# Kernel optimization log

Measured on AMD Instinct MI355X. Metric: run time of the kernel, lower is better.

The kernel has to match this reference:

```python
import jax, jax.numpy as jnp
import numpy as np

A, B, SDIM, ADIM, H, NH, DH = 15, 32768, 128, 32, 128, 4, 32
NEG = -1e9

def _lrelu(x):
    return jax.nn.leaky_relu(x, 0.01)

def setup_inputs() -> dict:
    key = jax.random.key(0)
    ks = jax.random.split(key, 14)
    w = lambda k, shp, s=0.05: jax.random.normal(k, shp, dtype=jnp.float32) * s
    return {
        'states': jax.random.normal(ks[0], (A, B, SDIM), dtype=jnp.float32),
        'actions': jax.random.normal(ks[1], (A, B, ADIM), dtype=jnp.float32),
        'Wenc': w(ks[2], (A, SDIM + ADIM, H)),
        'benc': w(ks[3], (A, H)),
        'Wsenc': w(ks[4], (A, SDIM, H)),
        'bsenc': w(ks[5], (A, H)),
        'Wk': w(ks[6], (NH, H, DH)),
        'Wsel': w(ks[7], (NH, H, DH)),
        'Wv': w(ks[8], (NH, H, DH)),
        'bv': w(ks[9], (NH, DH)),
        'Wc1': w(ks[10], (A, 2 * H, H)),
        'bc1': w(ks[11], (A, H)),
        'Wc2': w(ks[12], (A, H, ADIM)),
        'bc2': w(ks[13], (A, ADIM)),
    }

def reference(states, actions, Wenc, benc, Wsenc, bsenc, Wk, Wsel, Wv, bv, Wc1, bc1, Wc2, bc2):
    # per-agent (obs, act) encoders: [A,B,idim] x [A,idim,H] -> [A,B,H]
    sa = jnp.concatenate([states, actions], axis=-1)
    sa_enc = _lrelu(jnp.einsum('abi,aih->abh', sa, Wenc) + benc[:, None, :])
    s_enc = _lrelu(jnp.einsum('abs,ash->abh', states, Wsenc) + bsenc[:, None, :])
    # per-head key/value/selector projections (shared across agents)
    keys = jnp.einsum('jbe,ned->jbnd', sa_enc, Wk)                      # [A,B,NH,DH]
    vals = _lrelu(jnp.einsum('jbe,ned->jbnd', sa_enc, Wv) + bv[None, None])
    sel = jnp.einsum('ibe,ned->ibnd', s_enc, Wsel)                      # [A,B,NH,DH]
    # exclude-self attention over other agents
    logits = jnp.einsum('ibnd,jbnd->ibnj', sel, keys) / np.sqrt(DH).astype(np.float32)
    self_mask = jnp.eye(A, dtype=bool)[:, None, None, :]                # [A,1,1,A]
    probs = jax.nn.softmax(jnp.where(self_mask, NEG, logits), axis=-1)  # [A,B,NH,A]
    attn = jnp.einsum('ibnj,jbnd->ibnd', probs, vals)                   # [A,B,NH,DH]
    # per-agent critic head: cat(s_enc, all-head attention values) -> Q over actions
    critic_in = jnp.concatenate([s_enc, attn.reshape(A, B, NH * DH)], axis=-1)  # [A,B,2H]
    h = _lrelu(jnp.einsum('abi,aih->abh', critic_in, Wc1) + bc1[:, None, :])
    all_q = jnp.einsum('abh,aho->abo', h, Wc2) + bc2[:, None, :]        # [A,B,ADIM]
    return all_q
```

## Files before the change

kernel.cpp:

```cpp
#include <hip/hip_runtime.h>

typedef unsigned short u16;
typedef __attribute__((ext_vector_type(8))) short short8;
typedef __attribute__((ext_vector_type(4))) float f32x4;

#define NAG 15
#define NB 32768
#define NEG_BIG -1e30f

__device__ __forceinline__ u16 f2bf(float x){
  unsigned int u = __float_as_uint(x);
  u += 0x7fffu + ((u >> 16) & 1u);
  return (u16)(u >> 16);
}
__device__ __forceinline__ float bf2f(short h){
  return __uint_as_float(((unsigned int)(u16)h) << 16);
}

__global__ __launch_bounds__(256) void k0_conv(
    const float* __restrict__ Wenc, const float* __restrict__ Wsenc,
    const float* __restrict__ Wk, const float* __restrict__ Wsel, const float* __restrict__ Wv,
    const float* __restrict__ Wc1, const float* __restrict__ Wc2,
    u16* __restrict__ WencB, u16* __restrict__ WsencB,
    u16* __restrict__ WkB, u16* __restrict__ WvB, u16* __restrict__ WselB,
    u16* __restrict__ Wc1B, u16* __restrict__ Wc2B)
{
  int idx = blockIdx.x * 256 + threadIdx.x;
  if (idx < 307200){
    int a = idx / 20480, r = idx % 20480, n = r / 160, k = r % 160;
    WencB[idx] = f2bf(Wenc[a*20480 + k*128 + n]);
  } else if (idx < 552960){
    int i = idx - 307200; int a = i / 16384, r = i % 16384, n = r / 128, k = r % 128;
    WsencB[i] = f2bf(Wsenc[a*16384 + k*128 + n]);
  } else if (idx < 569344){
    int i = idx - 552960; int c = i / 128, k = i % 128;
    WkB[i] = f2bf(Wk[(c>>5)*4096 + k*32 + (c&31)]);
  } else if (idx < 585728){
    int i = idx - 569344; int c = i / 128, k = i % 128;
    WvB[i] = f2bf(Wv[(c>>5)*4096 + k*32 + (c&31)]);
  } else if (idx < 602112){
    int i = idx - 585728; int c = i / 128, k = i % 128;
    WselB[i] = f2bf(Wsel[(c>>5)*4096 + k*32 + (c&31)]);
  } else if (idx < 1093632){
    int i = idx - 602112; int a = i / 32768, r = i % 32768, n = r / 256, k = r % 256;
    Wc1B[i] = f2bf(Wc1[a*32768 + k*128 + n]);
  } else if (idx < 1155072){
    int i = idx - 1093632; int a = i / 4096, r = i % 4096, n = r / 128, k = r % 128;
    Wc2B[i] = f2bf(Wc2[a*4096 + k*32 + n]);
  }
}

__device__ __forceinline__ void mfma_block(const char* lds, int aOff, int aStride, int aMask,
    const u16* __restrict__ B, int bld, int ksteps,
    int m0, int c0, int l15, int l4, f32x4 acc[4][2])
{
  for (int ks = 0; ks < ksteps; ++ks){
    short8 af[4];
    #pragma unroll
    for (int fm = 0; fm < 4; ++fm){
      int row = m0 + fm*16 + l15;
      int slot = ks*4 + l4;
      af[fm] = *(const short8*)(lds + aOff + row*aStride + ((slot ^ (row & aMask)) << 4));
    }
    short8 bf[2];
    #pragma unroll
    for (int fn = 0; fn < 2; ++fn){
      int n = c0 + fn*16 + l15;
      bf[fn] = *(const short8*)(B + (size_t)n*bld + ks*32 + l4*8);
    }
    #pragma unroll
    for (int fm = 0; fm < 4; ++fm)
      #pragma unroll
      for (int fn = 0; fn < 2; ++fn)
        acc[fm][fn] = __builtin_amdgcn_mfma_f32_16x16x32_bf16(af[fm], bf[fn], acc[fm][fn], 0, 0, 0);
  }
}

__device__ __forceinline__ void epi_store(char* lds, f32x4 acc[4][2], const float* __restrict__ bias,
    bool act, int m0, int c0, int l15, int l4, int swzOff, int linOff)
{
  #pragma unroll
  for (int fm = 0; fm < 4; ++fm)
  #pragma unroll
  for (int fn = 0; fn < 2; ++fn){
    int col = c0 + fn*16 + l15;
    float bb = bias ? bias[col] : 0.0f;
    #pragma unroll
    for (int q = 0; q < 4; ++q){
      int row = m0 + fm*16 + l4*4 + q;
      float v = acc[fm][fn][q] + bb;
      if (act) v = v > 0.0f ? v : 0.01f * v;
      u16 h = f2bf(v);
      if (swzOff >= 0) *(u16*)(lds + swzOff + row*256 + (((col>>3) ^ (row&7))<<4) + ((col&7)<<1)) = h;
      if (linOff >= 0) *(u16*)(lds + linOff + row*256 + col*2) = h;
    }
  }
}

__device__ __forceinline__ void copy_out_bf16(const char* lds, int off, u16* __restrict__ dst,
                                              int a, int b0, int t)
{
  #pragma unroll
  for (int it = 0; it < 4; ++it){
    int e = t + it*512;
    int row = e >> 4, cb = e & 15;
    *(short8*)(dst + ((size_t)a*NB + b0 + row)*128 + cb*8) =
        *(const short8*)(lds + off + row*256 + cb*16);
  }
}

#define S_OFF 0
#define AC_OFF 32768
#define SA_OFF 40960
#define SE_OFF 73728
#define K1_LDS 106496

__global__ __launch_bounds__(512) void k1_enc(
    const float* __restrict__ states, const float* __restrict__ actions,
    const float* __restrict__ benc, const float* __restrict__ bsenc, const float* __restrict__ bvp,
    const u16* __restrict__ WencB, const u16* __restrict__ WsencB,
    const u16* __restrict__ WkB, const u16* __restrict__ WvB, const u16* __restrict__ WselB,
    u16* __restrict__ senc_g, u16* __restrict__ keys_g, u16* __restrict__ vals_g, u16* __restrict__ sel_g)
{
  extern __shared__ __align__(16) char lds[];
  const int a = blockIdx.y;
  const int b0 = blockIdx.x * 128;
  const int t = threadIdx.x;
  const int lane = t & 63, w = t >> 6;
  const int m0 = (w >> 2) * 64, c0 = (w & 3) * 32;
  const int l15 = lane & 15, l4 = lane >> 4;

  #pragma unroll
  for (int it = 0; it < 4; ++it){
    int e = t + it*512, row = e >> 4, cb = e & 15;
    const float* sp = states + ((size_t)a*NB + b0 + row)*128 + cb*8;
    float4 v0 = *(const float4*)sp, v1 = *(const float4*)(sp + 4);
    short8 p;
    p[0]=(short)f2bf(v0.x); p[1]=(short)f2bf(v0.y); p[2]=(short)f2bf(v0.z); p[3]=(short)f2bf(v0.w);
    p[4]=(short)f2bf(v1.x); p[5]=(short)f2bf(v1.y); p[6]=(short)f2bf(v1.z); p[7]=(short)f2bf(v1.w);
    *(short8*)(lds + S_OFF + row*256 + ((cb ^ (row&7))<<4)) = p;
  }
  {
    int row = t >> 2, cb = t & 3;
    const float* ap = actions + ((size_t)a*NB + b0 + row)*32 + cb*8;
    float4 v0 = *(const float4*)ap, v1 = *(const float4*)(ap + 4);
    short8 p;
    p[0]=(short)f2bf(v0.x); p[1]=(short)f2bf(v0.y); p[2]=(short)f2bf(v0.z); p[3]=(short)f2bf(v0.w);
    p[4]=(short)f2bf(v1.x); p[5]=(short)f2bf(v1.y); p[6]=(short)f2bf(v1.z); p[7]=(short)f2bf(v1.w);
    *(short8*)(lds + AC_OFF + row*64 + ((cb ^ (row&3))<<4)) = p;
  }
  __syncthreads();

  f32x4 acc[4][2];

  #pragma unroll
  for (int fm = 0; fm < 4; ++fm){ acc[fm][0] = (f32x4)0.0f; acc[fm][1] = (f32x4)0.0f; }
  mfma_block(lds, S_OFF, 256, 7, WencB + (size_t)a*20480, 160, 4, m0, c0, l15, l4, acc);
  {
    short8 af[4];
    #pragma unroll
    for (int fm = 0; fm < 4; ++fm){
      int row = m0 + fm*16 + l15;
      af[fm] = *(const short8*)(lds + AC_OFF + row*64 + ((l4 ^ (row&3))<<4));
    }
    short8 bf[2];
    #pragma unroll
    for (int fn = 0; fn < 2; ++fn){
      int n = c0 + fn*16 + l15;
      bf[fn] = *(const short8*)(WencB + (size_t)a*20480 + (size_t)n*160 + 128 + l4*8);
    }
    #pragma unroll
    for (int fm = 0; fm < 4; ++fm)
      #pragma unroll
      for (int fn = 0; fn < 2; ++fn)
        acc[fm][fn] = __builtin_amdgcn_mfma_f32_16x16x32_bf16(af[fm], bf[fn], acc[fm][fn], 0, 0, 0);
  }
  epi_store(lds, acc, benc + a*128, true, m0, c0, l15, l4, SA_OFF, -1);
  __syncthreads();

  #pragma unroll
  for (int fm = 0; fm < 4; ++fm){ acc[fm][0] = (f32x4)0.0f; acc[fm][1] = (f32x4)0.0f; }
  mfma_block(lds, S_OFF, 256, 7, WsencB + (size_t)a*16384, 128, 4, m0, c0, l15, l4, acc);
  __syncthreads();
  epi_store(lds, acc, bsenc + a*128, true, m0, c0, l15, l4, SE_OFF, 0);
  __syncthreads();
  copy_out_bf16(lds, 0, senc_g, a, b0, t);
  __syncthreads();

  #pragma unroll
  for (int fm = 0; fm < 4; ++fm){ acc[fm][0] = (f32x4)0.0f; acc[fm][1] = (f32x4)0.0f; }
  mfma_block(lds, SA_OFF, 256, 7, WkB, 128, 4, m0, c0, l15, l4, acc);
  epi_store(lds, acc, (const float*)nullptr, false, m0, c0, l15, l4, -1, 0);
  __syncthreads();
  copy_out_bf16(lds, 0, keys_g, a, b0, t);
  __syncthreads();

  #pragma unroll
  for (int fm = 0; fm < 4; ++fm){ acc[fm][0] = (f32x4)0.0f; acc[fm][1] = (f32x4)0.0f; }
  mfma_block(lds, SA_OFF, 256, 7, WvB, 128, 4, m0, c0, l15, l4, acc);
  epi_store(lds, acc, bvp, true, m0, c0, l15, l4, -1, 0);
  __syncthreads();
  copy_out_bf16(lds, 0, vals_g, a, b0, t);
  __syncthreads();

  #pragma unroll
  for (int fm = 0; fm < 4; ++fm){ acc[fm][0] = (f32x4)0.0f; acc[fm][1] = (f32x4)0.0f; }
  mfma_block(lds, SE_OFF, 256, 7, WselB, 128, 4, m0, c0, l15, l4, acc);
  epi_store(lds, acc, (const float*)nullptr, false, m0, c0, l15, l4, -1, 0);
  __syncthreads();
  copy_out_bf16(lds, 0, sel_g, a, b0, t);
}

#define K2A_LDS 130560

__global__ __launch_bounds__(512) void k2a_attn(
    const u16* __restrict__ keys_g, const u16* __restrict__ vals_g,
    const u16* __restrict__ sel_g, u16* __restrict__ attn_g)
{
  extern __shared__ __align__(16) char lds[];
  const int b0 = blockIdx.x * 16;
  const int t = threadIdx.x;
  for (int it = 0; it < 8; ++it){
    int e = t + it*512;
    if (e < 3840){
      int j = e >> 8, r = (e >> 4) & 15, c = e & 15;
      size_t src = ((size_t)j*NB + b0 + r)*128 + c*8;
      int dst = (j*16 + r)*272 + c*16;
      *(short8*)(lds + dst) = *(const short8*)(keys_g + src);
      *(short8*)(lds + 65280 + dst) = *(const short8*)(vals_g + src);
    }
  }
  __syncthreads();
  for (int e = t; e < 960; e += 512){
    int b = e & 15, n = (e >> 4) & 3, i = e >> 6;
    size_t base = ((size_t)i*NB + b0 + b)*128 + n*32;
    float sf[32];
    #pragma unroll
    for (int c4 = 0; c4 < 4; ++c4){
      short8 s8 = *(const short8*)(sel_g + base + c4*8);
      #pragma unroll
      for (int x = 0; x < 8; ++x) sf[c4*8+x] = bf2f(s8[x]);
    }
    float lg[15]; float mx = NEG_BIG;
    #pragma unroll
    for (int j = 0; j < 15; ++j){
      if (j == i){ lg[j] = NEG_BIG; continue; }
      int kb = (j*16 + b)*272 + n*64;
      float d = 0.f;
      #pragma unroll
      for (int c4 = 0; c4 < 4; ++c4){
        short8 k8 = *(const short8*)(lds + kb + c4*16);
        #pragma unroll
        for (int x = 0; x < 8; ++x) d += bf2f(k8[x]) * sf[c4*8+x];
      }
      d *= 0.17677669529663687f;
      lg[j] = d; mx = fmaxf(mx, d);
    }
    float sum = 0.f;
    #pragma unroll
    for (int j = 0; j < 15; ++j){
      float p = (j == i) ? 0.f : __expf(lg[j] - mx);
      lg[j] = p; sum += p;
    }
    float inv = 1.0f / sum;
    float oacc[32];
    #pragma unroll
    for (int x = 0; x < 32; ++x) oacc[x] = 0.f;
    #pragma unroll
    for (int j = 0; j < 15; ++j){
      if (j == i) continue;
      float p = lg[j];
      int vb = 65280 + (j*16 + b)*272 + n*64;
      #pragma unroll
      for (int c4 = 0; c4 < 4; ++c4){
        short8 v8 = *(const short8*)(lds + vb + c4*16);
        #pragma unroll
        for (int x = 0; x < 8; ++x) oacc[c4*8+x] += p * bf2f(v8[x]);
      }
    }
    #pragma unroll
    for (int c4 = 0; c4 < 4; ++c4){
      short8 o;
      #pragma unroll
      for (int x = 0; x < 8; ++x) o[x] = (short)f2bf(oacc[c4*8+x] * inv);
      *(short8*)(attn_g + base + c4*8) = o;
    }
  }
}

#define AIN_OFF 0
#define HL_OFF 65536
#define O2_OFF 98304
#define K2B_LDS 114688

__global__ __launch_bounds__(512) void k2b_critic(
    const u16* __restrict__ senc_g, const u16* __restrict__ attn_g,
    const u16* __restrict__ Wc1B, const u16* __restrict__ Wc2B,
    const float* __restrict__ bc1, const float* __restrict__ bc2,
    float* __restrict__ outp)
{
  extern __shared__ __align__(16) char lds[];
  const int a = blockIdx.y, b0 = blockIdx.x * 128, t = threadIdx.x;
  const int lane = t & 63, w = t >> 6;
  const int m0 = (w >> 2)*64, c0 = (w & 3)*32;
  const int l15 = lane & 15, l4 = lane >> 4;

  #pragma unroll
  for (int it = 0; it < 4; ++it){
    int e = t + it*512, row = e >> 4, cb = e & 15;
    size_t src = ((size_t)a*NB + b0 + row)*128 + cb*8;
    short8 v = *(const short8*)(senc_g + src);
    *(short8*)(lds + AIN_OFF + row*512 + ((cb ^ (row&7))<<4)) = v;
    short8 v2 = *(const short8*)(attn_g + src);
    *(short8*)(lds + AIN_OFF + row*512 + (((16 + cb) ^ (row&7))<<4)) = v2;
  }
  __syncthreads();

  f32x4 acc[4][2];
  #pragma unroll
  for (int fm = 0; fm < 4; ++fm){ acc[fm][0] = (f32x4)0.0f; acc[fm][1] = (f32x4)0.0f; }
  mfma_block(lds, AIN_OFF, 512, 7, Wc1B + (size_t)a*32768, 256, 8, m0, c0, l15, l4, acc);
  epi_store(lds, acc, bc1 + a*128, true, m0, c0, l15, l4, HL_OFF, -1);
  __syncthreads();

  const int r0 = (w >> 1)*32, cq = (w & 1)*16;
  f32x4 aq[2]; aq[0] = (f32x4)0.0f; aq[1] = (f32x4)0.0f;
  for (int ks = 0; ks < 4; ++ks){
    short8 af[2];
    #pragma unroll
    for (int fm = 0; fm < 2; ++fm){
      int row = r0 + fm*16 + l15, slot = ks*4 + l4;
      af[fm] = *(const short8*)(lds + HL_OFF + row*256 + ((slot ^ (row&7))<<4));
    }
    int n = cq + l15;
    short8 bq = *(const short8*)(Wc2B + (size_t)a*4096 + (size_t)n*128 + ks*32 + l4*8);
    aq[0] = __builtin_amdgcn_mfma_f32_16x16x32_bf16(af[0], bq, aq[0], 0, 0, 0);
    aq[1] = __builtin_amdgcn_mfma_f32_16x16x32_bf16(af[1], bq, aq[1], 0, 0, 0);
  }
  {
    int col = cq + l15; float bb = bc2[a*32 + col];
    #pragma unroll
    for (int fm = 0; fm < 2; ++fm)
      #pragma unroll
      for (int q = 0; q < 4; ++q){
        int row = r0 + fm*16 + l4*4 + q;
        *(float*)(lds + O2_OFF + (row*32 + col)*4) = aq[fm][q] + bb;
      }
  }
  __syncthreads();
  #pragma unroll
  for (int it = 0; it < 2; ++it){
    int e = t + it*512;
    float4 v = *(const float4*)(lds + O2_OFF + e*16);
    *(float4*)(outp + ((size_t)a*NB + b0 + (e>>3))*32 + (e&7)*4) = v;
  }
}

extern "C" void kernel_launch(void* const* d_in, const int* in_sizes, int n_in,
                              void* d_out, int out_size, void* d_ws, size_t ws_size,
                              hipStream_t stream)
{
  const float* states  = (const float*)d_in[0];
  const float* actions = (const float*)d_in[1];
  const float* Wenc    = (const float*)d_in[2];
  const float* benc    = (const float*)d_in[3];
  const float* Wsenc   = (const float*)d_in[4];
  const float* bsenc   = (const float*)d_in[5];
  const float* Wk      = (const float*)d_in[6];
  const float* Wsel    = (const float*)d_in[7];
  const float* Wv      = (const float*)d_in[8];
  const float* bv      = (const float*)d_in[9];
  const float* Wc1     = (const float*)d_in[10];
  const float* bc1     = (const float*)d_in[11];
  const float* Wc2     = (const float*)d_in[12];
  const float* bc2     = (const float*)d_in[13];

  char* ws = (char*)d_ws;
  u16* WencB  = (u16*)(ws + 0);
  u16* WsencB = (u16*)(ws + 614400);
  u16* WkB    = (u16*)(ws + 1105920);
  u16* WvB    = (u16*)(ws + 1138688);
  u16* WselB  = (u16*)(ws + 1171456);
  u16* Wc1B   = (u16*)(ws + 1204224);
  u16* Wc2B   = (u16*)(ws + 2187264);
  u16* senc_g = (u16*)(ws + 2310144);
  u16* keys_g = (u16*)(ws + 128139264);
  u16* vals_g = (u16*)(ws + 253968384);
  u16* sel_g  = (u16*)(ws + 379797504);
  if (ws_size < 505626624ULL) return;

  hipFuncSetAttribute((const void*)k1_enc,     hipFuncAttributeMaxDynamicSharedMemorySize, K1_LDS);
  hipFuncSetAttribute((const void*)k2a_attn,   hipFuncAttributeMaxDynamicSharedMemorySize, K2A_LDS);
  hipFuncSetAttribute((const void*)k2b_critic, hipFuncAttributeMaxDynamicSharedMemorySize, K2B_LDS);

  k0_conv<<<4512, 256, 0, stream>>>(Wenc, Wsenc, Wk, Wsel, Wv, Wc1, Wc2,
                                    WencB, WsencB, WkB, WvB, WselB, Wc1B, Wc2B);
  k1_enc<<<dim3(256, 15), 512, K1_LDS, stream>>>(states, actions, benc, bsenc, bv,
                                                 WencB, WsencB, WkB, WvB, WselB,
                                                 senc_g, keys_g, vals_g, sel_g);
  k2a_attn<<<2048, 512, K2A_LDS, stream>>>(keys_g, vals_g, sel_g, keys_g);
  k2b_critic<<<dim3(256, 15), 512, K2B_LDS, stream>>>(senc_g, keys_g, Wc1B, Wc2B,
                                                      bc1, bc2, (float*)d_out);
}
```

Measured before the change: 714.3 us.

## Fuse encoder, attention and critic into one kernel per 16-sample tile

Replaces the three-kernel pipeline (encoders, attention, critic) with a single kernel. Each 1024-thread block handles 16 batch rows across all 15 agents and keeps encodings, per-head keys, values, selectors and attention outputs in LDS. This removes roughly 500MB of bf16 intermediate global writes and reads. In exchange, weights are reloaded per small tile from global or L2, the block uses about 150KB of LDS (limiting occupancy), and the per-head loop adds many block barriers.

```diff
diff --git a/kernel.cpp b/kernel.cpp
--- a/kernel.cpp
+++ b/kernel.cpp
@@ -4,9 +4,7 @@
 typedef __attribute__((ext_vector_type(8))) short short8;
 typedef __attribute__((ext_vector_type(4))) float f32x4;
 
-#define NAG 15
 #define NB 32768
-#define NEG_BIG -1e30f
 
 __device__ __forceinline__ u16 f2bf(float x){
   unsigned int u = __float_as_uint(x);
@@ -15,6 +13,12 @@
 }
 __device__ __forceinline__ float bf2f(short h){
   return __uint_as_float(((unsigned int)(u16)h) << 16);
+}
+__device__ __forceinline__ short8 pack8(float4 a, float4 b){
+  short8 p;
+  p[0]=(short)f2bf(a.x); p[1]=(short)f2bf(a.y); p[2]=(short)f2bf(a.z); p[3]=(short)f2bf(a.w);
+  p[4]=(short)f2bf(b.x); p[5]=(short)f2bf(b.y); p[6]=(short)f2bf(b.z); p[7]=(short)f2bf(b.w);
+  return p;
 }
 
 __global__ __launch_bounds__(256) void k0_conv(
@@ -50,309 +54,291 @@
   }
 }
 
-__device__ __forceinline__ void mfma_block(const char* lds, int aOff, int aStride, int aMask,
-    const u16* __restrict__ B, int bld, int ksteps,
-    int m0, int c0, int l15, int l4, f32x4 acc[4][2])
-{
-  for (int ks = 0; ks < ksteps; ++ks){
-    short8 af[4];
-    #pragma unroll
-    for (int fm = 0; fm < 4; ++fm){
-      int row = m0 + fm*16 + l15;
-      int slot = ks*4 + l4;
-      af[fm] = *(const short8*)(lds + aOff + row*aStride + ((slot ^ (row & aMask)) << 4));
-    }
-    short8 bf[2];
-    #pragma unroll
-    for (int fn = 0; fn < 2; ++fn){
-      int n = c0 + fn*16 + l15;
-      bf[fn] = *(const short8*)(B + (size_t)n*bld + ks*32 + l4*8);
-    }
-    #pragma unroll
-    for (int fm = 0; fm < 4; ++fm)
-      #pragma unroll
-      for (int fn = 0; fn < 2; ++fn)
-        acc[fm][fn] = __builtin_amdgcn_mfma_f32_16x16x32_bf16(af[fm], bf[fn], acc[fm][fn], 0, 0, 0);
-  }
-}
-
-__device__ __forceinline__ void epi_store(char* lds, f32x4 acc[4][2], const float* __restrict__ bias,
-    bool act, int m0, int c0, int l15, int l4, int swzOff, int linOff)
-{
-  #pragma unroll
-  for (int fm = 0; fm < 4; ++fm)
-  #pragma unroll
-  for (int fn = 0; fn < 2; ++fn){
-    int col = c0 + fn*16 + l15;
-    float bb = bias ? bias[col] : 0.0f;
-    #pragma unroll
-    for (int q = 0; q < 4; ++q){
-      int row = m0 + fm*16 + l4*4 + q;
-      float v = acc[fm][fn][q] + bb;
-      if (act) v = v > 0.0f ? v : 0.01f * v;
-      u16 h = f2bf(v);
-      if (swzOff >= 0) *(u16*)(lds + swzOff + row*256 + (((col>>3) ^ (row&7))<<4) + ((col&7)<<1)) = h;
-      if (linOff >= 0) *(u16*)(lds + linOff + row*256 + col*2) = h;
-    }
-  }
-}
-
-__device__ __forceinline__ void copy_out_bf16(const char* lds, int off, u16* __restrict__ dst,
-                                              int a, int b0, int t)
-{
-  #pragma unroll
-  for (int it = 0; it < 4; ++it){
-    int e = t + it*512;
-    int row = e >> 4, cb = e & 15;
-    *(short8*)(dst + ((size_t)a*NB + b0 + row)*128 + cb*8) =
-        *(const short8*)(lds + off + row*256 + cb*16);
-  }
-}
-
-#define S_OFF 0
-#define AC_OFF 32768
-#define SA_OFF 40960
-#define SE_OFF 73728
-#define K1_LDS 106496
-
-__global__ __launch_bounds__(512) void k1_enc(
+#define R1 0
+#define R2 61440
+#define P1 122880
+#define P2 138240
+#define R3 122880
+#define K_LDS 153600
+
+__device__ __forceinline__ short8 ldA(const char* lds, int off, int row, int slot){
+  return *(const short8*)(lds + off + row*256 + ((slot ^ (row & 7)) << 4));
+}
+__device__ __forceinline__ void stSwz(char* lds, int off, int row, int col, u16 v){
+  *(u16*)(lds + off + row*256 + ((((col>>3) ^ (row&7))) << 4) + ((col&7) << 1)) = v;
+}
+
+#define MFMA(a8,b8,c) __builtin_amdgcn_mfma_f32_16x16x32_bf16(a8, b8, c, 0, 0, 0)
+
+__global__ __launch_bounds__(1024) void k_fused(
     const float* __restrict__ states, const float* __restrict__ actions,
     const float* __restrict__ benc, const float* __restrict__ bsenc, const float* __restrict__ bvp,
+    const float* __restrict__ bc1, const float* __restrict__ bc2,
     const u16* __restrict__ WencB, const u16* __restrict__ WsencB,
     const u16* __restrict__ WkB, const u16* __restrict__ WvB, const u16* __restrict__ WselB,
-    u16* __restrict__ senc_g, u16* __restrict__ keys_g, u16* __restrict__ vals_g, u16* __restrict__ sel_g)
-{
-  extern __shared__ __align__(16) char lds[];
-  const int a = blockIdx.y;
-  const int b0 = blockIdx.x * 128;
-  const int t = threadIdx.x;
-  const int lane = t & 63, w = t >> 6;
-  const int m0 = (w >> 2) * 64, c0 = (w & 3) * 32;
-  const int l15 = lane & 15, l4 = lane >> 4;
-
-  #pragma unroll
-  for (int it = 0; it < 4; ++it){
-    int e = t + it*512, row = e >> 4, cb = e & 15;
-    const float* sp = states + ((size_t)a*NB + b0 + row)*128 + cb*8;
-    float4 v0 = *(const float4*)sp, v1 = *(const float4*)(sp + 4);
-    short8 p;
-    p[0]=(short)f2bf(v0.x); p[1]=(short)f2bf(v0.y); p[2]=(short)f2bf(v0.z); p[3]=(short)f2bf(v0.w);
-    p[4]=(short)f2bf(v1.x); p[5]=(short)f2bf(v1.y); p[6]=(short)f2bf(v1.z); p[7]=(short)f2bf(v1.w);
-    *(short8*)(lds + S_OFF + row*256 + ((cb ^ (row&7))<<4)) = p;
-  }
-  {
-    int row = t >> 2, cb = t & 3;
-    const float* ap = actions + ((size_t)a*NB + b0 + row)*32 + cb*8;
-    float4 v0 = *(const float4*)ap, v1 = *(const float4*)(ap + 4);
-    short8 p;
-    p[0]=(short)f2bf(v0.x); p[1]=(short)f2bf(v0.y); p[2]=(short)f2bf(v0.z); p[3]=(short)f2bf(v0.w);
-    p[4]=(short)f2bf(v1.x); p[5]=(short)f2bf(v1.y); p[6]=(short)f2bf(v1.z); p[7]=(short)f2bf(v1.w);
-    *(short8*)(lds + AC_OFF + row*64 + ((cb ^ (row&3))<<4)) = p;
-  }
-  __syncthreads();
-
-  f32x4 acc[4][2];
-
-  #pragma unroll
-  for (int fm = 0; fm < 4; ++fm){ acc[fm][0] = (f32x4)0.0f; acc[fm][1] = (f32x4)0.0f; }
-  mfma_block(lds, S_OFF, 256, 7, WencB + (size_t)a*20480, 160, 4, m0, c0, l15, l4, acc);
-  {
-    short8 af[4];
-    #pragma unroll
-    for (int fm = 0; fm < 4; ++fm){
-      int row = m0 + fm*16 + l15;
-      af[fm] = *(const short8*)(lds + AC_OFF + row*64 + ((l4 ^ (row&3))<<4));
-    }
-    short8 bf[2];
-    #pragma unroll
-    for (int fn = 0; fn < 2; ++fn){
-      int n = c0 + fn*16 + l15;
-      bf[fn] = *(const short8*)(WencB + (size_t)a*20480 + (size_t)n*160 + 128 + l4*8);
-    }
-    #pragma unroll
-    for (int fm = 0; fm < 4; ++fm)
-      #pragma unroll
-      for (int fn = 0; fn < 2; ++fn)
-        acc[fm][fn] = __builtin_amdgcn_mfma_f32_16x16x32_bf16(af[fm], bf[fn], acc[fm][fn], 0, 0, 0);
-  }
-  epi_store(lds, acc, benc + a*128, true, m0, c0, l15, l4, SA_OFF, -1);
-  __syncthreads();
-
-  #pragma unroll
-  for (int fm = 0; fm < 4; ++fm){ acc[fm][0] = (f32x4)0.0f; acc[fm][1] = (f32x4)0.0f; }
-  mfma_block(lds, S_OFF, 256, 7, WsencB + (size_t)a*16384, 128, 4, m0, c0, l15, l4, acc);
-  __syncthreads();
-  epi_store(lds, acc, bsenc + a*128, true, m0, c0, l15, l4, SE_OFF, 0);
-  __syncthreads();
-  copy_out_bf16(lds, 0, senc_g, a, b0, t);
-  __syncthreads();
-
-  #pragma unroll
-  for (int fm = 0; fm < 4; ++fm){ acc[fm][0] = (f32x4)0.0f; acc[fm][1] = (f32x4)0.0f; }
-  mfma_block(lds, SA_OFF, 256, 7, WkB, 128, 4, m0, c0, l15, l4, acc);
-  epi_store(lds, acc, (const float*)nullptr, false, m0, c0, l15, l4, -1, 0);
-  __syncthreads();
-  copy_out_bf16(lds, 0, keys_g, a, b0, t);
-  __syncthreads();
-
-  #pragma unroll
-  for (int fm = 0; fm < 4; ++fm){ acc[fm][0] = (f32x4)0.0f; acc[fm][1] = (f32x4)0.0f; }
-  mfma_block(lds, SA_OFF, 256, 7, WvB, 128, 4, m0, c0, l15, l4, acc);
-  epi_store(lds, acc, bvp, true, m0, c0, l15, l4, -1, 0);
-  __syncthreads();
-  copy_out_bf16(lds, 0, vals_g, a, b0, t);
-  __syncthreads();
-
-  #pragma unroll
-  for (int fm = 0; fm < 4; ++fm){ acc[fm][0] = (f32x4)0.0f; acc[fm][1] = (f32x4)0.0f; }
-  mfma_block(lds, SE_OFF, 256, 7, WselB, 128, 4, m0, c0, l15, l4, acc);
-  epi_store(lds, acc, (const float*)nullptr, false, m0, c0, l15, l4, -1, 0);
-  __syncthreads();
-  copy_out_bf16(lds, 0, sel_g, a, b0, t);
-}
-
-#define K2A_LDS 130560
-
-__global__ __launch_bounds__(512) void k2a_attn(
-    const u16* __restrict__ keys_g, const u16* __restrict__ vals_g,
-    const u16* __restrict__ sel_g, u16* __restrict__ attn_g)
+    const u16* __restrict__ Wc1B, const u16* __restrict__ Wc2B,
+    float* __restrict__ outp)
 {
   extern __shared__ __align__(16) char lds[];
   const int b0 = blockIdx.x * 16;
   const int t = threadIdx.x;
-  for (int it = 0; it < 8; ++it){
-    int e = t + it*512;
-    if (e < 3840){
-      int j = e >> 8, r = (e >> 4) & 15, c = e & 15;
-      size_t src = ((size_t)j*NB + b0 + r)*128 + c*8;
-      int dst = (j*16 + r)*272 + c*16;
-      *(short8*)(lds + dst) = *(const short8*)(keys_g + src);
-      *(short8*)(lds + 65280 + dst) = *(const short8*)(vals_g + src);
-    }
-  }
-  __syncthreads();
-  for (int e = t; e < 960; e += 512){
-    int b = e & 15, n = (e >> 4) & 3, i = e >> 6;
-    size_t base = ((size_t)i*NB + b0 + b)*128 + n*32;
-    float sf[32];
+  const int lane = t & 63, w = t >> 6;
+  const int l15 = lane & 15, l4 = lane >> 4;
+
+  for (int c = t; c < 3840; c += 1024){
+    int row = c >> 4, cb = c & 15;
+    int ag = row >> 4, br = row & 15;
+    const float* sp = states + ((size_t)ag*NB + b0 + br)*128 + cb*8;
+    float4 v0 = *(const float4*)sp, v1 = *(const float4*)(sp + 4);
+    *(short8*)(lds + R2 + row*256 + ((cb ^ (row&7)) << 4)) = pack8(v0, v1);
+  }
+  __syncthreads();
+
+  #pragma unroll
+  for (int uu = 0; uu < 2; ++uu){
+    const int u = w + uu*16;
+    if (u < 30){
+      const int a = u >> 1, nh = u & 1;
+      f32x4 acc[4];
+      #pragma unroll
+      for (int fn = 0; fn < 4; ++fn) acc[fn] = (f32x4)0.0f;
+      const u16* Wb = WencB + (size_t)a*20480 + (size_t)(nh*64)*160;
+      for (int ks = 0; ks < 4; ++ks){
+        short8 a8 = ldA(lds, R2, a*16 + l15, ks*4 + l4);
+        #pragma unroll
+        for (int fn = 0; fn < 4; ++fn){
+          short8 b8 = *(const short8*)(Wb + (fn*16 + l15)*160 + ks*32 + l4*8);
+          acc[fn] = MFMA(a8, b8, acc[fn]);
+        }
+      }
+      {
+        const float* ap = actions + ((size_t)a*NB + b0 + l15)*32 + l4*8;
+        float4 u0 = *(const float4*)ap, u1 = *(const float4*)(ap + 4);
+        short8 a8 = pack8(u0, u1);
+        #pragma unroll
+        for (int fn = 0; fn < 4; ++fn){
+          short8 b8 = *(const short8*)(Wb + (fn*16 + l15)*160 + 128 + l4*8);
+          acc[fn] = MFMA(a8, b8, acc[fn]);
+        }
+      }
+      #pragma unroll
+      for (int fn = 0; fn < 4; ++fn){
+        int col = nh*64 + fn*16 + l15;
+        float bb = benc[a*128 + col];
+        #pragma unroll
+        for (int q = 0; q < 4; ++q){
+          int row = a*16 + l4*4 + q;
+          float v = acc[fn][q] + bb; v = v > 0.f ? v : 0.01f*v;
+          stSwz(lds, R1, row, col, f2bf(v));
+        }
+      }
+    }
+  }
+  f32x4 seacc[2][4];
+  #pragma unroll
+  for (int uu = 0; uu < 2; ++uu)
     #pragma unroll
-    for (int c4 = 0; c4 < 4; ++c4){
-      short8 s8 = *(const short8*)(sel_g + base + c4*8);
-      #pragma unroll
-      for (int x = 0; x < 8; ++x) sf[c4*8+x] = bf2f(s8[x]);
-    }
-    float lg[15]; float mx = NEG_BIG;
+    for (int fn = 0; fn < 4; ++fn) seacc[uu][fn] = (f32x4)0.0f;
+  #pragma unroll
+  for (int uu = 0; uu < 2; ++uu){
+    const int u = w + uu*16;
+    if (u < 30){
+      const int a = u >> 1, nh = u & 1;
+      const u16* Wb = WsencB + (size_t)a*16384 + (size_t)(nh*64)*128;
+      for (int ks = 0; ks < 4; ++ks){
+        short8 a8 = ldA(lds, R2, a*16 + l15, ks*4 + l4);
+        #pragma unroll
+        for (int fn = 0; fn < 4; ++fn){
+          short8 b8 = *(const short8*)(Wb + (fn*16 + l15)*128 + ks*32 + l4*8);
+          seacc[uu][fn] = MFMA(a8, b8, seacc[uu][fn]);
+        }
+      }
+    }
+  }
+  __syncthreads();
+  #pragma unroll
+  for (int uu = 0; uu < 2; ++uu){
+    const int u = w + uu*16;
+    if (u < 30){
+      const int a = u >> 1, nh = u & 1;
+      #pragma unroll
+      for (int fn = 0; fn < 4; ++fn){
+        int col = nh*64 + fn*16 + l15;
+        float bb = bsenc[a*128 + col];
+        #pragma unroll
+        for (int q = 0; q < 4; ++q){
+          int row = a*16 + l4*4 + q;
+          float v = seacc[uu][fn][q] + bb; v = v > 0.f ? v : 0.01f*v;
+          stSwz(lds, R2, row, col, f2bf(v));
+        }
+      }
+    }
+  }
+  __syncthreads();
+
+  f32x4 c1[8];
+  #pragma unroll
+  for (int fn = 0; fn < 8; ++fn) c1[fn] = (f32x4)0.0f;
+  if (w < 15){
+    for (int ks = 0; ks < 4; ++ks){
+      short8 a8 = ldA(lds, R2, w*16 + l15, ks*4 + l4);
+      #pragma unroll
+      for (int fn = 0; fn < 8; ++fn){
+        short8 b8 = *(const short8*)(Wc1B + (size_t)w*32768 + (fn*16 + l15)*256 + ks*32 + l4*8);
+        c1[fn] = MFMA(a8, b8, c1[fn]);
+      }
+    }
+  }
+
+  for (int h = 0; h < 4; ++h){
+    float pb[15]; float inv = 0.f;
     #pragma unroll
-    for (int j = 0; j < 15; ++j){
-      if (j == i){ lg[j] = NEG_BIG; continue; }
-      int kb = (j*16 + b)*272 + n*64;
-      float d = 0.f;
-      #pragma unroll
-      for (int c4 = 0; c4 < 4; ++c4){
-        short8 k8 = *(const short8*)(lds + kb + c4*16);
-        #pragma unroll
-        for (int x = 0; x < 8; ++x) d += bf2f(k8[x]) * sf[c4*8+x];
-      }
-      d *= 0.17677669529663687f;
-      lg[j] = d; mx = fmaxf(mx, d);
-    }
-    float sum = 0.f;
+    for (int uu = 0; uu < 2; ++uu){
+      const int u = w + uu*16;
+      if (u < 30){
+        const int m = u >> 1, nf = u & 1;
+        f32x4 as = (f32x4)0.0f, ak = (f32x4)0.0f;
+        const int nrow = h*32 + nf*16 + l15;
+        for (int ks = 0; ks < 4; ++ks){
+          short8 a2 = ldA(lds, R2, m*16 + l15, ks*4 + l4);
+          short8 a1 = ldA(lds, R1, m*16 + l15, ks*4 + l4);
+          short8 bs = *(const short8*)(WselB + (size_t)nrow*128 + ks*32 + l4*8);
+          short8 bk = *(const short8*)(WkB   + (size_t)nrow*128 + ks*32 + l4*8);
+          as = MFMA(a2, bs, as);
+          ak = MFMA(a1, bk, ak);
+        }
+        #pragma unroll
+        for (int q = 0; q < 4; ++q){
+          int row = m*16 + l4*4 + q, col = nf*16 + l15;
+          *(u16*)(lds + P2 + row*64 + col*2) = f2bf(as[q]);
+          *(u16*)(lds + P1 + row*64 + col*2) = f2bf(ak[q]);
+        }
+      }
+    }
+    __syncthreads();
+    if (w < 15){
+      const int bq = lane >> 2, l = lane & 3;
+      const int qrow = w*16 + bq;
+      short8 s8 = *(const short8*)(lds + P2 + qrow*64 + l*16);
+      float sf[8];
+      #pragma unroll
+      for (int x = 0; x < 8; ++x) sf[x] = bf2f(s8[x]);
+      #pragma unroll
+      for (int j = 0; j < 15; ++j){
+        short8 k8 = *(const short8*)(lds + P1 + (j*16 + bq)*64 + l*16);
+        float d = 0.f;
+        #pragma unroll
+        for (int x = 0; x < 8; ++x) d += bf2f(k8[x]) * sf[x];
+        d += __shfl_xor(d, 1);
+        d += __shfl_xor(d, 2);
+        pb[j] = d * 0.17677669529663687f;
+      }
+      float mx = -1e30f;
+      #pragma unroll
+      for (int j = 0; j < 15; ++j) if (j != w) mx = fmaxf(mx, pb[j]);
+      float sum = 0.f;
+      #pragma unroll
+      for (int j = 0; j < 15; ++j){
+        float p = (j == w) ? 0.f : __expf(pb[j] - mx);
+        pb[j] = p; sum += p;
+      }
+      inv = 1.f / sum;
+    }
+    __syncthreads();
     #pragma unroll
-    for (int j = 0; j < 15; ++j){
-      float p = (j == i) ? 0.f : __expf(lg[j] - mx);
-      lg[j] = p; sum += p;
-    }
-    float inv = 1.0f / sum;
-    float oacc[32];
+    for (int uu = 0; uu < 2; ++uu){
+      const int u = w + uu*16;
+      if (u < 30){
+        const int m = u >> 1, nf = u & 1;
+        f32x4 av = (f32x4)0.0f;
+        const int nrow = h*32 + nf*16 + l15;
+        for (int ks = 0; ks < 4; ++ks){
+          short8 a1 = ldA(lds, R1, m*16 + l15, ks*4 + l4);
+          short8 b8 = *(const short8*)(WvB + (size_t)nrow*128 + ks*32 + l4*8);
+          av = MFMA(a1, b8, av);
+        }
+        int col = nf*16 + l15;
+        float bb = bvp[h*32 + col];
+        #pragma unroll
+        for (int q = 0; q < 4; ++q){
+          int row = m*16 + l4*4 + q;
+          float v = av[q] + bb; v = v > 0.f ? v : 0.01f*v;
+          *(u16*)(lds + P2 + row*64 + col*2) = f2bf(v);
+        }
+      }
+    }
+    __syncthreads();
+    if (w < 15){
+      const int bq = lane >> 2, l = lane & 3;
+      const int qrow = w*16 + bq;
+      float oa[8];
+      #pragma unroll
+      for (int x = 0; x < 8; ++x) oa[x] = 0.f;
+      #pragma unroll
+      for (int j = 0; j < 15; ++j){
+        if (j == w) continue;
+        float p = pb[j];
+        short8 v8 = *(const short8*)(lds + P2 + (j*16 + bq)*64 + l*16);
+        #pragma unroll
+        for (int x = 0; x < 8; ++x) oa[x] += p * bf2f(v8[x]);
+      }
+      short8 o;
+      #pragma unroll
+      for (int x = 0; x < 8; ++x) o[x] = (short)f2bf(oa[x] * inv);
+      *(short8*)(lds + P1 + qrow*64 + l*16) = o;
+    }
+    __syncthreads();
+    if (w < 15){
+      short8 a8 = *(const short8*)(lds + P1 + (w*16 + l15)*64 + l4*16);
+      #pragma unroll
+      for (int fn = 0; fn < 8; ++fn){
+        short8 b8 = *(const short8*)(Wc1B + (size_t)w*32768 + (fn*16 + l15)*256 + 128 + h*32 + l4*8);
+        c1[fn] = MFMA(a8, b8, c1[fn]);
+      }
+    }
+    __syncthreads();
+  }
+
+  if (w < 15){
     #pragma unroll
-    for (int x = 0; x < 32; ++x) oacc[x] = 0.f;
-    #pragma unroll
-    for (int j = 0; j < 15; ++j){
-      if (j == i) continue;
-      float p = lg[j];
-      int vb = 65280 + (j*16 + b)*272 + n*64;
-      #pragma unroll
-      for (int c4 = 0; c4 < 4; ++c4){
-        short8 v8 = *(const short8*)(lds + vb + c4*16);
-        #pragma unroll
-        for (int x = 0; x < 8; ++x) oacc[c4*8+x] += p * bf2f(v8[x]);
-      }
-    }
-    #pragma unroll
-    for (int c4 = 0; c4 < 4; ++c4){
-      short8 o;
-      #pragma unroll
-      for (int x = 0; x < 8; ++x) o[x] = (short)f2bf(oacc[c4*8+x] * inv);
-      *(short8*)(attn_g + base + c4*8) = o;
-    }
-  }
-}
-
-#define AIN_OFF 0
-#define HL_OFF 65536
-#define O2_OFF 98304
-#define K2B_LDS 114688
-
-__global__ __launch_bounds__(512) void k2b_critic(
-    const u16* __restrict__ senc_g, const u16* __restrict__ attn_g,
-    const u16* __restrict__ Wc1B, const u16* __restrict__ Wc2B,
-    const float* __restrict__ bc1, const float* __restrict__ bc2,
-    float* __restrict__ outp)
-{
-  extern __shared__ __align__(16) char lds[];
-  const int a = blockIdx.y, b0 = blockIdx.x * 128, t = threadIdx.x;
-  const int lane = t & 63, w = t >> 6;
-  const int m0 = (w >> 2)*64, c0 = (w & 3)*32;
-  const int l15 = lane & 15, l4 = lane >> 4;
-
-  #pragma unroll
-  for (int it = 0; it < 4; ++it){
-    int e = t + it*512, row = e >> 4, cb = e & 15;
-    size_t src = ((size_t)a*NB + b0 + row)*128 + cb*8;
-    short8 v = *(const short8*)(senc_g + src);
-    *(short8*)(lds + AIN_OFF + row*512 + ((cb ^ (row&7))<<4)) = v;
-    short8 v2 = *(const short8*)(attn_g + src);
-    *(short8*)(lds + AIN_OFF + row*512 + (((16 + cb) ^ (row&7))<<4)) = v2;
-  }
-  __syncthreads();
-
-  f32x4 acc[4][2];
-  #pragma unroll
-  for (int fm = 0; fm < 4; ++fm){ acc[fm][0] = (f32x4)0.0f; acc[fm][1] = (f32x4)0.0f; }
-  mfma_block(lds, AIN_OFF, 512, 7, Wc1B + (size_t)a*32768, 256, 8, m0, c0, l15, l4, acc);
-  epi_store(lds, acc, bc1 + a*128, true, m0, c0, l15, l4, HL_OFF, -1);
-  __syncthreads();
-
-  const int r0 = (w >> 1)*32, cq = (w & 1)*16;
-  f32x4 aq[2]; aq[0] = (f32x4)0.0f; aq[1] = (f32x4)0.0f;
-  for (int ks = 0; ks < 4; ++ks){
-    short8 af[2];
-    #pragma unroll
-    for (int fm = 0; fm < 2; ++fm){
-      int row = r0 + fm*16 + l15, slot = ks*4 + l4;
-      af[fm] = *(const short8*)(lds + HL_OFF + row*256 + ((slot ^ (row&7))<<4));
-    }
-    int n = cq + l15;
-    short8 bq = *(const short8*)(Wc2B + (size_t)a*4096 + (size_t)n*128 + ks*32 + l4*8);
-    aq[0] = __builtin_amdgcn_mfma_f32_16x16x32_bf16(af[0], bq, aq[0], 0, 0, 0);
-    aq[1] = __builtin_amdgcn_mfma_f32_16x16x32_bf16(af[1], bq, aq[1], 0, 0, 0);
-  }
-  {
-    int col = cq + l15; float bb = bc2[a*32 + col];
-    #pragma unroll
-    for (int fm = 0; fm < 2; ++fm)
+    for (int fn = 0; fn < 8; ++fn){
+      int col = fn*16 + l15;
+      float bb = bc1[w*128 + col];
       #pragma unroll
       for (int q = 0; q < 4; ++q){
-        int row = r0 + fm*16 + l4*4 + q;
-        *(float*)(lds + O2_OFF + (row*32 + col)*4) = aq[fm][q] + bb;
-      }
-  }
-  __syncthreads();
-  #pragma unroll
-  for (int it = 0; it < 2; ++it){
-    int e = t + it*512;
-    float4 v = *(const float4*)(lds + O2_OFF + e*16);
-    *(float4*)(outp + ((size_t)a*NB + b0 + (e>>3))*32 + (e&7)*4) = v;
+        int row = w*16 + l4*4 + q;
+        float v = c1[fn][q] + bb; v = v > 0.f ? v : 0.01f*v;
+        stSwz(lds, R2, row, col, f2bf(v));
+      }
+    }
+  }
+  __syncthreads();
+
+  #pragma unroll
+  for (int uu = 0; uu < 2; ++uu){
+    const int u = w + uu*16;
+    if (u < 30){
+      const int m = u >> 1, nf = u & 1;
+      f32x4 a2 = (f32x4)0.0f;
+      for (int ks = 0; ks < 4; ++ks){
+        short8 a8 = ldA(lds, R2, m*16 + l15, ks*4 + l4);
+        short8 b8 = *(const short8*)(Wc2B + (size_t)m*4096 + (nf*16 + l15)*128 + ks*32 + l4*8);
+        a2 = MFMA(a8, b8, a2);
+      }
+      int col = nf*16 + l15;
+      float bb = bc2[m*32 + col];
+      #pragma unroll
+      for (int q = 0; q < 4; ++q){
+        int row = m*16 + l4*4 + q;
+        *(float*)(lds + R3 + row*128 + col*4) = a2[q] + bb;
+      }
+    }
+  }
+  __syncthreads();
+  for (int e = t; e < 1920; e += 1024){
+    f32x4 v = *(const f32x4*)(lds + R3 + e*16);
+    int row = e >> 3, c4 = e & 7;
+    *(f32x4*)(outp + ((size_t)(row >> 4)*NB + b0 + (row & 15))*32 + c4*4) = v;
   }
 }
 
@@ -383,22 +369,13 @@
   u16* WselB  = (u16*)(ws + 1171456);
   u16* Wc1B   = (u16*)(ws + 1204224);
   u16* Wc2B   = (u16*)(ws + 2187264);
-  u16* senc_g = (u16*)(ws + 2310144);
-  u16* keys_g = (u16*)(ws + 128139264);
-  u16* vals_g = (u16*)(ws + 253968384);
-  u16* sel_g  = (u16*)(ws + 379797504);
-  if (ws_size < 505626624ULL) return;
-
-  hipFuncSetAttribute((const void*)k1_enc,     hipFuncAttributeMaxDynamicSharedMemorySize, K1_LDS);
-  hipFuncSetAttribute((const void*)k2a_attn,   hipFuncAttributeMaxDynamicSharedMemorySize, K2A_LDS);
-  hipFuncSetAttribute((const void*)k2b_critic, hipFuncAttributeMaxDynamicSharedMemorySize, K2B_LDS);
+  if (ws_size < 2310144ULL) return;
+
+  hipFuncSetAttribute((const void*)k_fused, hipFuncAttributeMaxDynamicSharedMemorySize, K_LDS);
 
   k0_conv<<<4512, 256, 0, stream>>>(Wenc, Wsenc, Wk, Wsel, Wv, Wc1, Wc2,
                                     WencB, WsencB, WkB, WvB, WselB, Wc1B, Wc2B);
-  k1_enc<<<dim3(256, 15), 512, K1_LDS, stream>>>(states, actions, benc, bsenc, bv,
-                                                 WencB, WsencB, WkB, WvB, WselB,
-                                                 senc_g, keys_g, vals_g, sel_g);
-  k2a_attn<<<2048, 512, K2A_LDS, stream>>>(keys_g, vals_g, sel_g, keys_g);
-  k2b_critic<<<dim3(256, 15), 512, K2B_LDS, stream>>>(senc_g, keys_g, Wc1B, Wc2B,
-                                                      bc1, bc2, (float*)d_out);
-}
+  k_fused<<<2048, 1024, K_LDS, stream>>>(states, actions, benc, bsenc, bv, bc1, bc2,
+                                         WencB, WsencB, WkB, WvB, WselB, Wc1B, Wc2B,
+                                         (float*)d_out);
+}
```

Result: slower. 994.1 us (+39.2%).
